# Performance work log

Hardware: AMD Instinct MI355X
Metric: run time of the kernel (lower is better)

Reference implementation:

```python
import jax, jax.numpy as jnp
import numpy as np

NUM_HEADS = 16
HEAD_DIM = 64  # hidden_size 1024 / 16 heads


def setup_inputs() -> dict:
    key = jax.random.key(0)
    ks = jax.random.split(key, 4)
    B, S, H = 2, 2048, 1024
    scale = 1.0 / np.sqrt(H)
    return {
        "hidden_states": jax.random.normal(ks[0], (B, S, H), dtype=jnp.float32),
        "attention_mask": jnp.zeros((B, 1, 1, S), dtype=jnp.float32),
        "Wq": jax.random.normal(ks[1], (H, H), dtype=jnp.float32) * scale,
        "bq": jnp.zeros((H,), dtype=jnp.float32),
        "Wk": jax.random.normal(ks[2], (H, H), dtype=jnp.float32) * scale,
        "bk": jnp.zeros((H,), dtype=jnp.float32),
        "Wv": jax.random.normal(ks[3], (H, H), dtype=jnp.float32) * scale,
        "bv": jnp.zeros((H,), dtype=jnp.float32),
    }


def reference(hidden_states, attention_mask, Wq, bq, Wk, bk, Wv, bv):
    B, S, H = hidden_states.shape
    h, d = NUM_HEADS, HEAD_DIM

    def heads(x):  # [B,S,H] -> [B,h,S,d]
        return x.reshape(B, S, h, d).transpose(0, 2, 1, 3)

    q = heads(hidden_states @ Wq + bq)
    k = heads(hidden_states @ Wk + bk)
    v = heads(hidden_states @ Wv + bv)

    # [B,h,S,S] scores, scaled then additive-masked (HF BERT semantics)
    scores = jnp.einsum("bhqd,bhkd->bhqk", q, k) / jnp.sqrt(jnp.float32(d))
    scores = scores + attention_mask
    probs = jax.nn.softmax(scores, axis=-1)  # dropout p=0 -> identity

    ctx = jnp.einsum("bhqk,bhkd->bhqd", probs, v)
    ctx = ctx.transpose(0, 2, 1, 3).reshape(B, S, H)
    return ctx
```

## Files before the change

### kernel.cpp

```cpp
#include <hip/hip_runtime.h>
#include <hip/hip_bf16.h>


#define SEQ   2048
#define HID   1024
#define NHEAD 16
#define HD    64
#define SD    ((size_t)SEQ * HD)

typedef __bf16 bf16x8 __attribute__((ext_vector_type(8)));
typedef float  f32x4  __attribute__((ext_vector_type(4)));

#define L2E 1.4426950408889634f
#define SOFT_OFF 16.0f

__device__ __forceinline__ unsigned short f2b(float f) {
    unsigned int x = __float_as_uint(f);
    x += 0x7FFFu + ((x >> 16) & 1u);
    return (unsigned short)(x >> 16);
}

__global__ __launch_bounds__(256) void cvt_x_k(const float* __restrict__ X,
                                               unsigned short* __restrict__ Xb)
{
    const size_t i = ((size_t)blockIdx.x * 256 + threadIdx.x) * 4;
    const float4 v = *(const float4*)(X + i);
    ushort4 o;
    o.x = f2b(v.x); o.y = f2b(v.y); o.z = f2b(v.z); o.w = f2b(v.w);
    *(ushort4*)(Xb + i) = o;
}

__global__ __launch_bounds__(256) void cvt_w_k(
    const float* __restrict__ Wq, const float* __restrict__ Wk,
    const float* __restrict__ Wv, unsigned short* __restrict__ Wtb)
{
    __shared__ __align__(16) unsigned short T[64][68];
    const int z = blockIdx.z;
    const float* __restrict__ W = (z == 0) ? Wq : (z == 1) ? Wk : Wv;
    const int k0 = blockIdx.x * 64, n0 = blockIdx.y * 64;
    const int tid = threadIdx.x;
    #pragma unroll
    for (int it = 0; it < 16; ++it) {
        const int idx = 256 * it + tid;
        const int r = idx >> 6, c = idx & 63;
        T[c][r] = f2b(W[(size_t)(k0 + r) * HID + n0 + c]);
    }
    __syncthreads();
    unsigned short* dst = Wtb + (size_t)z * HID * HID;
    #pragma unroll
    for (int it = 0; it < 4; ++it) {
        const int idx = 256 * it + tid;
        const int n = idx >> 4, c4 = (idx & 15) * 4;
        *(ushort4*)(dst + (size_t)(n0 + n) * HID + k0 + c4) = *(ushort4*)&T[n][c4];
    }
}

__device__ __forceinline__ void gemm_epilogue(
    f32x4 acc[4][4], const float* __restrict__ Bp,
    unsigned short* __restrict__ scratch, unsigned short (*Et)[68],
    int z, int m0, int n0, int wr, int wc, int ln, int quad)
{
    const int b = m0 >> 11;
    const int srow0 = (m0 + wr) & (SEQ - 1);
    const int head = (n0 + wc) >> 6;
    __syncthreads();

    if (z == 2) {
        #pragma unroll
        for (int half = 0; half < 2; ++half) {
            #pragma unroll
            for (int nt2 = 0; nt2 < 2; ++nt2) {
                const int nt = half * 2 + nt2;
                const float bias = Bp[n0 + wc + nt * 16 + ln];
                #pragma unroll
                for (int mt = 0; mt < 4; ++mt) {
                    ushort4 o;
                    o.x = f2b(acc[mt][nt][0] + bias);
                    o.y = f2b(acc[mt][nt][1] + bias);
                    o.z = f2b(acc[mt][nt][2] + bias);
                    o.w = f2b(acc[mt][nt][3] + bias);
                    *(ushort4*)&Et[nt2 * 16 + ln][mt * 16 + quad * 4] = o;
                }
            }
            __syncthreads();
            #pragma unroll
            for (int it = 0; it < 8; ++it) {
                const int d = it * 4 + quad, s4 = ln * 4;
                *(ushort4*)(scratch +
                    ((size_t)(64 + b * NHEAD + head) * HD + half * 32 + d) * SEQ
                    + srow0 + s4) = *(const ushort4*)&Et[d][s4];
            }
            __syncthreads();
        }
    } else {
        #pragma unroll
        for (int half = 0; half < 2; ++half) {
            #pragma unroll
            for (int mt2 = 0; mt2 < 2; ++mt2) {
                const int mt = half * 2 + mt2;
                #pragma unroll
                for (int nt = 0; nt < 4; ++nt) {
                    const float bias = Bp[n0 + wc + nt * 16 + ln];
                    #pragma unroll
                    for (int r = 0; r < 4; ++r)
                        Et[mt2 * 16 + quad * 4 + r][nt * 16 + ln] =
                            f2b(acc[mt][nt][r] + bias);
                }
            }
            __syncthreads();
            #pragma unroll
            for (int it = 0; it < 8; ++it) {
                const int r = it * 4 + quad, c4 = ln * 4;
                *(ushort4*)(scratch +
                    ((size_t)(z * 32 + b * NHEAD + head) * SEQ + srow0
                     + half * 32 + r) * HD + c4) = *(const ushort4*)&Et[r][c4];
            }
            __syncthreads();
        }
    }
}

__global__ __launch_bounds__(256) void qkv_gemm_bf16(
    const unsigned short* __restrict__ Xb, const unsigned short* __restrict__ Wtb,
    const float* __restrict__ bq, const float* __restrict__ bk,
    const float* __restrict__ bv, unsigned short* __restrict__ scratch)
{
    __shared__ __align__(16) unsigned char pool[20480];
    unsigned short (*Xs)[40] = (unsigned short (*)[40])pool;
    unsigned short (*Wt)[40] = (unsigned short (*)[40])(pool + 10240);

    const int z = blockIdx.z;
    const float* __restrict__ Bp = (z == 0) ? bq : (z == 1) ? bk : bv;
    const unsigned short* __restrict__ Wz = Wtb + (size_t)z * HID * HID;

    const int tid = threadIdx.x, w = tid >> 6, lane = tid & 63;
    const int ln = lane & 15, quad = lane >> 4;
    const int wr = (w >> 1) * 64, wc = (w & 1) * 64;
    const int m0 = blockIdx.x * 128, n0 = blockIdx.y * 128;
    const int sr = tid >> 2, c8 = (tid & 3) * 8;

    f32x4 acc[4][4];
    #pragma unroll
    for (int i = 0; i < 4; ++i)
        #pragma unroll
        for (int j = 0; j < 4; ++j) acc[i][j] = (f32x4){0.f, 0.f, 0.f, 0.f};

    uint4 xg0 = *(const uint4*)(Xb + (size_t)(m0 + sr) * HID + c8);
    uint4 xg1 = *(const uint4*)(Xb + (size_t)(m0 + sr + 64) * HID + c8);
    uint4 wg0 = *(const uint4*)(Wz + (size_t)(n0 + sr) * HID + c8);
    uint4 wg1 = *(const uint4*)(Wz + (size_t)(n0 + sr + 64) * HID + c8);

    for (int k0 = 0; k0 < HID; k0 += 32) {
        __syncthreads();
        *(uint4*)&Xs[sr][c8]      = xg0;
        *(uint4*)&Xs[sr + 64][c8] = xg1;
        *(uint4*)&Wt[sr][c8]      = wg0;
        *(uint4*)&Wt[sr + 64][c8] = wg1;
        __syncthreads();
        const int kn = (k0 + 32) & (HID - 1);
        xg0 = *(const uint4*)(Xb + (size_t)(m0 + sr) * HID + kn + c8);
        xg1 = *(const uint4*)(Xb + (size_t)(m0 + sr + 64) * HID + kn + c8);
        wg0 = *(const uint4*)(Wz + (size_t)(n0 + sr) * HID + kn + c8);
        wg1 = *(const uint4*)(Wz + (size_t)(n0 + sr + 64) * HID + kn + c8);

        bf16x8 am[4], bn[4];
        #pragma unroll
        for (int t = 0; t < 4; ++t) {
            am[t] = *(const bf16x8*)&Xs[wr + t * 16 + ln][quad * 8];
            bn[t] = *(const bf16x8*)&Wt[wc + t * 16 + ln][quad * 8];
        }
        #pragma unroll
        for (int mt = 0; mt < 4; ++mt)
            #pragma unroll
            for (int nt = 0; nt < 4; ++nt)
                acc[mt][nt] = __builtin_amdgcn_mfma_f32_16x16x32_bf16(
                    am[mt], bn[nt], acc[mt][nt], 0, 0, 0);
    }
    unsigned short (*Et)[68] = (unsigned short (*)[68])(pool + (size_t)w * 4352);
    gemm_epilogue(acc, Bp, scratch, Et, z, m0, n0, wr, wc, ln, quad);
}

__global__ __launch_bounds__(256) void qkv_gemm_fp32(
    const float* __restrict__ X,
    const float* __restrict__ Wq, const float* __restrict__ bq,
    const float* __restrict__ Wk, const float* __restrict__ bk,
    const float* __restrict__ Wv, const float* __restrict__ bv,
    unsigned short* __restrict__ scratch)
{
    __shared__ __align__(16) unsigned char pool[20480];
    unsigned short (*Xs)[40] = (unsigned short (*)[40])pool;
    unsigned short (*Wt)[40] = (unsigned short (*)[40])(pool + 10240);

    const int z = blockIdx.z;
    const float* __restrict__ W  = (z == 0) ? Wq : (z == 1) ? Wk : Wv;
    const float* __restrict__ Bp = (z == 0) ? bq : (z == 1) ? bk : bv;

    const int tid = threadIdx.x, w = tid >> 6, lane = tid & 63;
    const int ln = lane & 15, quad = lane >> 4;
    const int wr = (w >> 1) * 64, wc = (w & 1) * 64;
    const int m0 = blockIdx.x * 128, n0 = blockIdx.y * 128;

    const int xr = tid >> 3, xc = (tid & 7) * 4;
    const int wkr = tid >> 5, wnc = (tid & 31) * 4;

    f32x4 acc[4][4];
    #pragma unroll
    for (int i = 0; i < 4; ++i)
        #pragma unroll
        for (int j = 0; j < 4; ++j) acc[i][j] = (f32x4){0.f, 0.f, 0.f, 0.f};

    for (int k0 = 0; k0 < HID; k0 += 32) {
        __syncthreads();
        #pragma unroll
        for (int it = 0; it < 4; ++it) {
            const int r = xr + 32 * it;
            const float4 xv = *(const float4*)(X + (size_t)(m0 + r) * HID + k0 + xc);
            ushort4 xb;
            xb.x = f2b(xv.x); xb.y = f2b(xv.y); xb.z = f2b(xv.z); xb.w = f2b(xv.w);
            *(ushort4*)&Xs[r][xc] = xb;
            const int kr = wkr + 8 * it;
            const float4 wv = *(const float4*)(W + (size_t)(k0 + kr) * HID + n0 + wnc);
            Wt[wnc + 0][kr] = f2b(wv.x);
            Wt[wnc + 1][kr] = f2b(wv.y);
            Wt[wnc + 2][kr] = f2b(wv.z);
            Wt[wnc + 3][kr] = f2b(wv.w);
        }
        __syncthreads();
        bf16x8 am[4], bn[4];
        #pragma unroll
        for (int t = 0; t < 4; ++t) {
            am[t] = *(const bf16x8*)&Xs[wr + t * 16 + ln][quad * 8];
            bn[t] = *(const bf16x8*)&Wt[wc + t * 16 + ln][quad * 8];
        }
        #pragma unroll
        for (int mt = 0; mt < 4; ++mt)
            #pragma unroll
            for (int nt = 0; nt < 4; ++nt)
                acc[mt][nt] = __builtin_amdgcn_mfma_f32_16x16x32_bf16(
                    am[mt], bn[nt], acc[mt][nt], 0, 0, 0);
    }
    unsigned short (*Et)[68] = (unsigned short (*)[68])(pool + (size_t)w * 4352);
    gemm_epilogue(acc, Bp, scratch, Et, z, m0, n0, wr, wc, ln, quad);
}

__global__ __launch_bounds__(256) void attn_mfma(
    const unsigned short* __restrict__ scratch,
    const float* __restrict__ mask,
    float* __restrict__ out)
{
    __shared__ __align__(16) unsigned char smem[46080];
    unsigned short (*Ks)[64][72] = (unsigned short (*)[64][72])smem;
    unsigned short (*Vt)[64][72] = (unsigned short (*)[64][72])(smem + 18432);
    unsigned short (*Ps)[72]     = (unsigned short (*)[72])(smem + 36864);
    float (*Obuf)[68] = (float (*)[68])smem;

    const int orig = blockIdx.x;
    const int wg = ((orig & 7) << 7) + (orig >> 3);
    const int qt = wg & 31;
    const int bh = wg >> 5;
    const int b = bh >> 4, head = bh & 15;

    const unsigned short* __restrict__ Qp  = scratch + (size_t)bh * SD;
    const unsigned short* __restrict__ Kp  = scratch + (size_t)(32 + bh) * SD;
    const unsigned short* __restrict__ Vtp = scratch + (size_t)(64 + bh) * SD;
    const float* __restrict__ maskp = mask + b * SEQ;

    const int tid = threadIdx.x, w = tid >> 6, lane = tid & 63;
    const int ln = lane & 15, quad = lane >> 4;

    const int qrow = qt * 64 + w * 16 + ln;
    const bf16x8 qb0 = *(const bf16x8*)(Qp + (size_t)qrow * HD + quad * 8);
    const bf16x8 qb1 = *(const bf16x8*)(Qp + (size_t)qrow * HD + 32 + quad * 8);

    f32x4 O[4];
    #pragma unroll
    for (int t = 0; t < 4; ++t) O[t] = (f32x4){0.f, 0.f, 0.f, 0.f};
    float lr = 0.0f;

    const int sr8 = tid >> 3, sc8 = (tid & 7) * 8;

    {
        uint4 a = *(const uint4*)(Kp + (size_t)sr8 * HD + sc8);
        uint4 c = *(const uint4*)(Kp + (size_t)(sr8 + 32) * HD + sc8);
        uint4 d = *(const uint4*)(Vtp + (size_t)sr8 * SEQ + sc8);
        uint4 e = *(const uint4*)(Vtp + (size_t)(sr8 + 32) * SEQ + sc8);
        *(uint4*)&Ks[0][sr8][sc8]      = a;
        *(uint4*)&Ks[0][sr8 + 32][sc8] = c;
        *(uint4*)&Vt[0][sr8][sc8]      = d;
        *(uint4*)&Vt[0][sr8 + 32][sc8] = e;
    }
    uint4 kg0 = *(const uint4*)(Kp + (size_t)(64 + sr8) * HD + sc8);
    uint4 kg1 = *(const uint4*)(Kp + (size_t)(64 + sr8 + 32) * HD + sc8);
    uint4 vg0 = *(const uint4*)(Vtp + (size_t)sr8 * SEQ + 64 + sc8);
    uint4 vg1 = *(const uint4*)(Vtp + (size_t)(sr8 + 32) * SEQ + 64 + sc8);
    __syncthreads();

    for (int kt = 0; kt < 32; ++kt) {
        const int cur = kt & 1;
        if (kt < 31) {
            *(uint4*)&Ks[cur ^ 1][sr8][sc8]      = kg0;
            *(uint4*)&Ks[cur ^ 1][sr8 + 32][sc8] = kg1;
            *(uint4*)&Vt[cur ^ 1][sr8][sc8]      = vg0;
            *(uint4*)&Vt[cur ^ 1][sr8 + 32][sc8] = vg1;
        }
        if (kt < 30) {
            const int kn = kt + 2;
            kg0 = *(const uint4*)(Kp + (size_t)(kn * 64 + sr8) * HD + sc8);
            kg1 = *(const uint4*)(Kp + (size_t)(kn * 64 + sr8 + 32) * HD + sc8);
            vg0 = *(const uint4*)(Vtp + (size_t)sr8 * SEQ + kn * 64 + sc8);
            vg1 = *(const uint4*)(Vtp + (size_t)(sr8 + 32) * SEQ + kn * 64 + sc8);
        }

        f32x4 s[4];
        #pragma unroll
        for (int t = 0; t < 4; ++t) {
            const bf16x8 ka0 = *(const bf16x8*)&Ks[cur][t * 16 + ln][quad * 8];
            const bf16x8 ka1 = *(const bf16x8*)&Ks[cur][t * 16 + ln][32 + quad * 8];
            f32x4 a = (f32x4){0.f, 0.f, 0.f, 0.f};
            a = __builtin_amdgcn_mfma_f32_16x16x32_bf16(ka0, qb0, a, 0, 0, 0);
            a = __builtin_amdgcn_mfma_f32_16x16x32_bf16(ka1, qb1, a, 0, 0, 0);
            s[t] = a;
        }

        const float c = 0.125f * L2E;
        #pragma unroll
        for (int t = 0; t < 4; ++t) {
            const float4 mk4 = *(const float4*)(maskp + kt * 64 + t * 16 + quad * 4);
            const float b0 = fmaf(mk4.x, L2E, -SOFT_OFF);
            const float b1 = fmaf(mk4.y, L2E, -SOFT_OFF);
            const float b2 = fmaf(mk4.z, L2E, -SOFT_OFF);
            const float b3 = fmaf(mk4.w, L2E, -SOFT_OFF);
            const float p0 = exp2f(fmaf(s[t][0], c, b0));
            const float p1 = exp2f(fmaf(s[t][1], c, b1));
            const float p2 = exp2f(fmaf(s[t][2], c, b2));
            const float p3 = exp2f(fmaf(s[t][3], c, b3));
            lr += (p0 + p1) + (p2 + p3);
            unsigned int w0, w1;
            asm("v_cvt_pk_bf16_f32 %0, %1, %2" : "=v"(w0) : "v"(p0), "v"(p1));
            asm("v_cvt_pk_bf16_f32 %0, %1, %2" : "=v"(w1) : "v"(p2), "v"(p3));
            uint2 pw; pw.x = w0; pw.y = w1;
            *(uint2*)&Ps[w * 16 + ln][t * 16 + quad * 4] = pw;
        }

        const bf16x8 pb0 = *(const bf16x8*)&Ps[w * 16 + ln][quad * 8];
        const bf16x8 pb1 = *(const bf16x8*)&Ps[w * 16 + ln][32 + quad * 8];
        #pragma unroll
        for (int t = 0; t < 4; ++t) {
            const bf16x8 va0 = *(const bf16x8*)&Vt[cur][t * 16 + ln][quad * 8];
            const bf16x8 va1 = *(const bf16x8*)&Vt[cur][t * 16 + ln][32 + quad * 8];
            O[t] = __builtin_amdgcn_mfma_f32_16x16x32_bf16(va0, pb0, O[t], 0, 0, 0);
            O[t] = __builtin_amdgcn_mfma_f32_16x16x32_bf16(va1, pb1, O[t], 0, 0, 0);
        }

        __syncthreads();
    }

    lr += __shfl_xor(lr, 16);
    lr += __shfl_xor(lr, 32);

    const float inv = 1.0f / lr;
    #pragma unroll
    for (int t = 0; t < 4; ++t) {
        float4 o4;
        o4.x = O[t][0] * inv; o4.y = O[t][1] * inv;
        o4.z = O[t][2] * inv; o4.w = O[t][3] * inv;
        *(float4*)&Obuf[w * 16 + ln][t * 16 + quad * 4] = o4;
    }
    __syncthreads();
    #pragma unroll
    for (int it = 0; it < 4; ++it) {
        const int r = (tid >> 4) + 16 * it, c4 = (tid & 15) * 4;
        *(float4*)(out + ((size_t)b * SEQ + qt * 64 + r) * HID + head * HD + c4)
            = *(const float4*)&Obuf[r][c4];
    }
}

extern "C" void kernel_launch(void* const* d_in, const int* in_sizes, int n_in,
                              void* d_out, int out_size, void* d_ws, size_t ws_size,
                              hipStream_t stream) {
    const float* X    = (const float*)d_in[0];
    const float* mask = (const float*)d_in[1];
    const float* Wq   = (const float*)d_in[2];
    const float* bq   = (const float*)d_in[3];
    const float* Wk   = (const float*)d_in[4];
    const float* bk   = (const float*)d_in[5];
    const float* Wv   = (const float*)d_in[6];
    const float* bv   = (const float*)d_in[7];

    unsigned short* scratch = (unsigned short*)d_ws;
    float* out = (float*)d_out;

    const bool big = (ws_size >= (40ull << 20));
    if (big) {
        unsigned short* Xb  = scratch + 96 * SD;
        unsigned short* Wtb = Xb + (size_t)2 * SEQ * HID;
        cvt_x_k<<<4096, 256, 0, stream>>>(X, Xb);
        cvt_w_k<<<dim3(16, 16, 3), 256, 0, stream>>>(Wq, Wk, Wv, Wtb);
        qkv_gemm_bf16<<<dim3(32, 8, 3), 256, 0, stream>>>(
            Xb, Wtb, bq, bk, bv, scratch);
    } else {
        qkv_gemm_fp32<<<dim3(32, 8, 3), 256, 0, stream>>>(
            X, Wq, bq, Wk, bk, Wv, bv, scratch);
    }
    attn_mfma<<<1024, 256, 0, stream>>>(scratch, mask, out);
}
```

Measured before the change: 214.8 us.

## Process two key tiles per iteration in attention loop with batched prefetch

```diff
diff --git a/kernel.cpp b/kernel.cpp
--- a/kernel.cpp
+++ b/kernel.cpp
@@ -248,10 +248,10 @@
     const float* __restrict__ mask,
     float* __restrict__ out)
 {
-    __shared__ __align__(16) unsigned char smem[46080];
+    __shared__ __align__(16) unsigned char smem[55296];
     unsigned short (*Ks)[64][72] = (unsigned short (*)[64][72])smem;
     unsigned short (*Vt)[64][72] = (unsigned short (*)[64][72])(smem + 18432);
-    unsigned short (*Ps)[72]     = (unsigned short (*)[72])(smem + 36864);
+    unsigned short (*Ps)[64][72] = (unsigned short (*)[64][72])(smem + 36864);
     float (*Obuf)[68] = (float (*)[68])smem;
 
     const int orig = blockIdx.x;
@@ -279,50 +279,50 @@
 
     const int sr8 = tid >> 3, sc8 = (tid & 7) * 8;
 
-    {
-        uint4 a = *(const uint4*)(Kp + (size_t)sr8 * HD + sc8);
-        uint4 c = *(const uint4*)(Kp + (size_t)(sr8 + 32) * HD + sc8);
-        uint4 d = *(const uint4*)(Vtp + (size_t)sr8 * SEQ + sc8);
-        uint4 e = *(const uint4*)(Vtp + (size_t)(sr8 + 32) * SEQ + sc8);
-        *(uint4*)&Ks[0][sr8][sc8]      = a;
-        *(uint4*)&Ks[0][sr8 + 32][sc8] = c;
-        *(uint4*)&Vt[0][sr8][sc8]      = d;
-        *(uint4*)&Vt[0][sr8 + 32][sc8] = e;
-    }
-    uint4 kg0 = *(const uint4*)(Kp + (size_t)(64 + sr8) * HD + sc8);
-    uint4 kg1 = *(const uint4*)(Kp + (size_t)(64 + sr8 + 32) * HD + sc8);
-    uint4 vg0 = *(const uint4*)(Vtp + (size_t)sr8 * SEQ + 64 + sc8);
-    uint4 vg1 = *(const uint4*)(Vtp + (size_t)(sr8 + 32) * SEQ + 64 + sc8);
+    #pragma unroll
+    for (int tp = 0; tp < 2; ++tp) {
+        uint4 a = *(const uint4*)(Kp + (size_t)(tp * 64 + sr8) * HD + sc8);
+        uint4 c = *(const uint4*)(Kp + (size_t)(tp * 64 + sr8 + 32) * HD + sc8);
+        uint4 d = *(const uint4*)(Vtp + (size_t)sr8 * SEQ + tp * 64 + sc8);
+        uint4 e = *(const uint4*)(Vtp + (size_t)(sr8 + 32) * SEQ + tp * 64 + sc8);
+        *(uint4*)&Ks[tp][sr8][sc8]      = a;
+        *(uint4*)&Ks[tp][sr8 + 32][sc8] = c;
+        *(uint4*)&Vt[tp][sr8][sc8]      = d;
+        *(uint4*)&Vt[tp][sr8 + 32][sc8] = e;
+    }
+    uint4 kgA0 = *(const uint4*)(Kp + (size_t)(2 * 64 + sr8) * HD + sc8);
+    uint4 kgA1 = *(const uint4*)(Kp + (size_t)(2 * 64 + sr8 + 32) * HD + sc8);
+    uint4 vgA0 = *(const uint4*)(Vtp + (size_t)sr8 * SEQ + 2 * 64 + sc8);
+    uint4 vgA1 = *(const uint4*)(Vtp + (size_t)(sr8 + 32) * SEQ + 2 * 64 + sc8);
+    uint4 kgB0 = *(const uint4*)(Kp + (size_t)(3 * 64 + sr8) * HD + sc8);
+    uint4 kgB1 = *(const uint4*)(Kp + (size_t)(3 * 64 + sr8 + 32) * HD + sc8);
+    uint4 vgB0 = *(const uint4*)(Vtp + (size_t)sr8 * SEQ + 3 * 64 + sc8);
+    uint4 vgB1 = *(const uint4*)(Vtp + (size_t)(sr8 + 32) * SEQ + 3 * 64 + sc8);
     __syncthreads();
 
-    for (int kt = 0; kt < 32; ++kt) {
-        const int cur = kt & 1;
-        if (kt < 31) {
-            *(uint4*)&Ks[cur ^ 1][sr8][sc8]      = kg0;
-            *(uint4*)&Ks[cur ^ 1][sr8 + 32][sc8] = kg1;
-            *(uint4*)&Vt[cur ^ 1][sr8][sc8]      = vg0;
-            *(uint4*)&Vt[cur ^ 1][sr8 + 32][sc8] = vg1;
-        }
-        if (kt < 30) {
-            const int kn = kt + 2;
-            kg0 = *(const uint4*)(Kp + (size_t)(kn * 64 + sr8) * HD + sc8);
-            kg1 = *(const uint4*)(Kp + (size_t)(kn * 64 + sr8 + 32) * HD + sc8);
-            vg0 = *(const uint4*)(Vtp + (size_t)sr8 * SEQ + kn * 64 + sc8);
-            vg1 = *(const uint4*)(Vtp + (size_t)(sr8 + 32) * SEQ + kn * 64 + sc8);
-        }
-
-        f32x4 s[4];
-        #pragma unroll
-        for (int t = 0; t < 4; ++t) {
-            const bf16x8 ka0 = *(const bf16x8*)&Ks[cur][t * 16 + ln][quad * 8];
-            const bf16x8 ka1 = *(const bf16x8*)&Ks[cur][t * 16 + ln][32 + quad * 8];
+    const float cc = 0.125f * L2E;
+
+    for (int kt = 0; kt < 32; kt += 2) {
+        f32x4 sA[4], sB[4];
+        #pragma unroll
+        for (int t = 0; t < 4; ++t) {
+            const bf16x8 ka0 = *(const bf16x8*)&Ks[0][t * 16 + ln][quad * 8];
+            const bf16x8 ka1 = *(const bf16x8*)&Ks[0][t * 16 + ln][32 + quad * 8];
             f32x4 a = (f32x4){0.f, 0.f, 0.f, 0.f};
             a = __builtin_amdgcn_mfma_f32_16x16x32_bf16(ka0, qb0, a, 0, 0, 0);
             a = __builtin_amdgcn_mfma_f32_16x16x32_bf16(ka1, qb1, a, 0, 0, 0);
-            s[t] = a;
-        }
-
-        const float c = 0.125f * L2E;
+            sA[t] = a;
+        }
+        #pragma unroll
+        for (int t = 0; t < 4; ++t) {
+            const bf16x8 kb0 = *(const bf16x8*)&Ks[1][t * 16 + ln][quad * 8];
+            const bf16x8 kb1 = *(const bf16x8*)&Ks[1][t * 16 + ln][32 + quad * 8];
+            f32x4 a = (f32x4){0.f, 0.f, 0.f, 0.f};
+            a = __builtin_amdgcn_mfma_f32_16x16x32_bf16(kb0, qb0, a, 0, 0, 0);
+            a = __builtin_amdgcn_mfma_f32_16x16x32_bf16(kb1, qb1, a, 0, 0, 0);
+            sB[t] = a;
+        }
+
         #pragma unroll
         for (int t = 0; t < 4; ++t) {
             const float4 mk4 = *(const float4*)(maskp + kt * 64 + t * 16 + quad * 4);
@@ -330,28 +330,81 @@
             const float b1 = fmaf(mk4.y, L2E, -SOFT_OFF);
             const float b2 = fmaf(mk4.z, L2E, -SOFT_OFF);
             const float b3 = fmaf(mk4.w, L2E, -SOFT_OFF);
-            const float p0 = exp2f(fmaf(s[t][0], c, b0));
-            const float p1 = exp2f(fmaf(s[t][1], c, b1));
-            const float p2 = exp2f(fmaf(s[t][2], c, b2));
-            const float p3 = exp2f(fmaf(s[t][3], c, b3));
+            const float p0 = exp2f(fmaf(sA[t][0], cc, b0));
+            const float p1 = exp2f(fmaf(sA[t][1], cc, b1));
+            const float p2 = exp2f(fmaf(sA[t][2], cc, b2));
+            const float p3 = exp2f(fmaf(sA[t][3], cc, b3));
             lr += (p0 + p1) + (p2 + p3);
             unsigned int w0, w1;
             asm("v_cvt_pk_bf16_f32 %0, %1, %2" : "=v"(w0) : "v"(p0), "v"(p1));
             asm("v_cvt_pk_bf16_f32 %0, %1, %2" : "=v"(w1) : "v"(p2), "v"(p3));
             uint2 pw; pw.x = w0; pw.y = w1;
-            *(uint2*)&Ps[w * 16 + ln][t * 16 + quad * 4] = pw;
-        }
-
-        const bf16x8 pb0 = *(const bf16x8*)&Ps[w * 16 + ln][quad * 8];
-        const bf16x8 pb1 = *(const bf16x8*)&Ps[w * 16 + ln][32 + quad * 8];
-        #pragma unroll
-        for (int t = 0; t < 4; ++t) {
-            const bf16x8 va0 = *(const bf16x8*)&Vt[cur][t * 16 + ln][quad * 8];
-            const bf16x8 va1 = *(const bf16x8*)&Vt[cur][t * 16 + ln][32 + quad * 8];
-            O[t] = __builtin_amdgcn_mfma_f32_16x16x32_bf16(va0, pb0, O[t], 0, 0, 0);
-            O[t] = __builtin_amdgcn_mfma_f32_16x16x32_bf16(va1, pb1, O[t], 0, 0, 0);
-        }
-
+            *(uint2*)&Ps[0][w * 16 + ln][t * 16 + quad * 4] = pw;
+        }
+        #pragma unroll
+        for (int t = 0; t < 4; ++t) {
+            const float4 mk4 = *(const float4*)(maskp + (kt + 1) * 64 + t * 16 + quad * 4);
+            const float b0 = fmaf(mk4.x, L2E, -SOFT_OFF);
+            const float b1 = fmaf(mk4.y, L2E, -SOFT_OFF);
+            const float b2 = fmaf(mk4.z, L2E, -SOFT_OFF);
+            const float b3 = fmaf(mk4.w, L2E, -SOFT_OFF);
+            const float p0 = exp2f(fmaf(sB[t][0], cc, b0));
+            const float p1 = exp2f(fmaf(sB[t][1], cc, b1));
+            const float p2 = exp2f(fmaf(sB[t][2], cc, b2));
+            const float p3 = exp2f(fmaf(sB[t][3], cc, b3));
+            lr += (p0 + p1) + (p2 + p3);
+            unsigned int w0, w1;
+            asm("v_cvt_pk_bf16_f32 %0, %1, %2" : "=v"(w0) : "v"(p0), "v"(p1));
+            asm("v_cvt_pk_bf16_f32 %0, %1, %2" : "=v"(w1) : "v"(p2), "v"(p3));
+            uint2 pw; pw.x = w0; pw.y = w1;
+            *(uint2*)&Ps[1][w * 16 + ln][t * 16 + quad * 4] = pw;
+        }
+
+        {
+            const bf16x8 pb0 = *(const bf16x8*)&Ps[0][w * 16 + ln][quad * 8];
+            const bf16x8 pb1 = *(const bf16x8*)&Ps[0][w * 16 + ln][32 + quad * 8];
+            #pragma unroll
+            for (int t = 0; t < 4; ++t) {
+                const bf16x8 va0 = *(const bf16x8*)&Vt[0][t * 16 + ln][quad * 8];
+                const bf16x8 va1 = *(const bf16x8*)&Vt[0][t * 16 + ln][32 + quad * 8];
+                O[t] = __builtin_amdgcn_mfma_f32_16x16x32_bf16(va0, pb0, O[t], 0, 0, 0);
+                O[t] = __builtin_amdgcn_mfma_f32_16x16x32_bf16(va1, pb1, O[t], 0, 0, 0);
+            }
+        }
+        {
+            const bf16x8 pb0 = *(const bf16x8*)&Ps[1][w * 16 + ln][quad * 8];
+            const bf16x8 pb1 = *(const bf16x8*)&Ps[1][w * 16 + ln][32 + quad * 8];
+            #pragma unroll
+            for (int t = 0; t < 4; ++t) {
+                const bf16x8 va0 = *(const bf16x8*)&Vt[1][t * 16 + ln][quad * 8];
+                const bf16x8 va1 = *(const bf16x8*)&Vt[1][t * 16 + ln][32 + quad * 8];
+                O[t] = __builtin_amdgcn_mfma_f32_16x16x32_bf16(va0, pb0, O[t], 0, 0, 0);
+                O[t] = __builtin_amdgcn_mfma_f32_16x16x32_bf16(va1, pb1, O[t], 0, 0, 0);
+            }
+        }
+
+        __syncthreads();
+        if (kt < 30) {
+            *(uint4*)&Ks[0][sr8][sc8]      = kgA0;
+            *(uint4*)&Ks[0][sr8 + 32][sc8] = kgA1;
+            *(uint4*)&Vt[0][sr8][sc8]      = vgA0;
+            *(uint4*)&Vt[0][sr8 + 32][sc8] = vgA1;
+            *(uint4*)&Ks[1][sr8][sc8]      = kgB0;
+            *(uint4*)&Ks[1][sr8 + 32][sc8] = kgB1;
+            *(uint4*)&Vt[1][sr8][sc8]      = vgB0;
+            *(uint4*)&Vt[1][sr8 + 32][sc8] = vgB1;
+            if (kt < 28) {
+                const int ka = kt + 4, kb = kt + 5;
+                kgA0 = *(const uint4*)(Kp + (size_t)(ka * 64 + sr8) * HD + sc8);
+                kgA1 = *(const uint4*)(Kp + (size_t)(ka * 64 + sr8 + 32) * HD + sc8);
+                vgA0 = *(const uint4*)(Vtp + (size_t)sr8 * SEQ + ka * 64 + sc8);
+                vgA1 = *(const uint4*)(Vtp + (size_t)(sr8 + 32) * SEQ + ka * 64 + sc8);
+                kgB0 = *(const uint4*)(Kp + (size_t)(kb * 64 + sr8) * HD + sc8);
+                kgB1 = *(const uint4*)(Kp + (size_t)(kb * 64 + sr8 + 32) * HD + sc8);
+                vgB0 = *(const uint4*)(Vtp + (size_t)sr8 * SEQ + kb * 64 + sc8);
+                vgB1 = *(const uint4*)(Vtp + (size_t)(sr8 + 32) * SEQ + kb * 64 + sc8);
+            }
+        }
         __syncthreads();
     }
 
```

After: 216.4 us. About the same (+0.7%).

## Use direct global-to-LDS loads with double buffering in QKV bf16 GEMM

Applied to the files above, without the earlier changes.

```diff
diff --git a/kernel.cpp b/kernel.cpp
--- a/kernel.cpp
+++ b/kernel.cpp
@@ -18,6 +18,13 @@
     unsigned int x = __float_as_uint(f);
     x += 0x7FFFu + ((x >> 16) & 1u);
     return (unsigned short)(x >> 16);
+}
+
+__device__ __forceinline__ void gload16(const unsigned short* g,
+                                        unsigned short* l) {
+    __builtin_amdgcn_global_load_lds(
+        (const __attribute__((address_space(1))) unsigned int*)g,
+        (__attribute__((address_space(3))) unsigned int*)l, 16, 0, 0);
 }
 
 __global__ __launch_bounds__(256) void cvt_x_k(const float* __restrict__ X,
@@ -125,9 +132,7 @@
     const float* __restrict__ bq, const float* __restrict__ bk,
     const float* __restrict__ bv, unsigned short* __restrict__ scratch)
 {
-    __shared__ __align__(16) unsigned char pool[20480];
-    unsigned short (*Xs)[40] = (unsigned short (*)[40])pool;
-    unsigned short (*Wt)[40] = (unsigned short (*)[40])(pool + 10240);
+    __shared__ __align__(16) unsigned short pool[2][2][128][32];
 
     const int z = blockIdx.z;
     const float* __restrict__ Bp = (z == 0) ? bq : (z == 1) ? bk : bv;
@@ -137,7 +142,10 @@
     const int ln = lane & 15, quad = lane >> 4;
     const int wr = (w >> 1) * 64, wc = (w & 1) * 64;
     const int m0 = blockIdx.x * 128, n0 = blockIdx.y * 128;
-    const int sr = tid >> 2, c8 = (tid & 3) * 8;
+
+    const int L0 = w * 128 + lane;
+    const int r0 = L0 >> 2,        c0 = (L0 & 3) * 8;
+    const int r1 = (L0 + 64) >> 2, c1 = ((L0 + 64) & 3) * 8;
 
     f32x4 acc[4][4];
     #pragma unroll
@@ -145,29 +153,33 @@
         #pragma unroll
         for (int j = 0; j < 4; ++j) acc[i][j] = (f32x4){0.f, 0.f, 0.f, 0.f};
 
-    uint4 xg0 = *(const uint4*)(Xb + (size_t)(m0 + sr) * HID + c8);
-    uint4 xg1 = *(const uint4*)(Xb + (size_t)(m0 + sr + 64) * HID + c8);
-    uint4 wg0 = *(const uint4*)(Wz + (size_t)(n0 + sr) * HID + c8);
-    uint4 wg1 = *(const uint4*)(Wz + (size_t)(n0 + sr + 64) * HID + c8);
-
+    {
+        unsigned short* lx = &pool[0][0][0][0] + (size_t)(w * 128) * 8;
+        unsigned short* lw = &pool[0][1][0][0] + (size_t)(w * 128) * 8;
+        gload16(Xb + (size_t)(m0 + r0) * HID + c0, lx);
+        gload16(Xb + (size_t)(m0 + r1) * HID + c1, lx + 64 * 8);
+        gload16(Wz + (size_t)(n0 + r0) * HID + c0, lw);
+        gload16(Wz + (size_t)(n0 + r1) * HID + c1, lw + 64 * 8);
+    }
+
+    int cur = 0;
     for (int k0 = 0; k0 < HID; k0 += 32) {
         __syncthreads();
-        *(uint4*)&Xs[sr][c8]      = xg0;
-        *(uint4*)&Xs[sr + 64][c8] = xg1;
-        *(uint4*)&Wt[sr][c8]      = wg0;
-        *(uint4*)&Wt[sr + 64][c8] = wg1;
-        __syncthreads();
-        const int kn = (k0 + 32) & (HID - 1);
-        xg0 = *(const uint4*)(Xb + (size_t)(m0 + sr) * HID + kn + c8);
-        xg1 = *(const uint4*)(Xb + (size_t)(m0 + sr + 64) * HID + kn + c8);
-        wg0 = *(const uint4*)(Wz + (size_t)(n0 + sr) * HID + kn + c8);
-        wg1 = *(const uint4*)(Wz + (size_t)(n0 + sr + 64) * HID + kn + c8);
+        if (k0 + 32 < HID) {
+            const int kn = k0 + 32, nxt = cur ^ 1;
+            unsigned short* lx = &pool[nxt][0][0][0] + (size_t)(w * 128) * 8;
+            unsigned short* lw = &pool[nxt][1][0][0] + (size_t)(w * 128) * 8;
+            gload16(Xb + (size_t)(m0 + r0) * HID + kn + c0, lx);
+            gload16(Xb + (size_t)(m0 + r1) * HID + kn + c1, lx + 64 * 8);
+            gload16(Wz + (size_t)(n0 + r0) * HID + kn + c0, lw);
+            gload16(Wz + (size_t)(n0 + r1) * HID + kn + c1, lw + 64 * 8);
+        }
 
         bf16x8 am[4], bn[4];
         #pragma unroll
         for (int t = 0; t < 4; ++t) {
-            am[t] = *(const bf16x8*)&Xs[wr + t * 16 + ln][quad * 8];
-            bn[t] = *(const bf16x8*)&Wt[wc + t * 16 + ln][quad * 8];
+            am[t] = *(const bf16x8*)&pool[cur][0][wr + t * 16 + ln][quad * 8];
+            bn[t] = *(const bf16x8*)&pool[cur][1][wc + t * 16 + ln][quad * 8];
         }
         #pragma unroll
         for (int mt = 0; mt < 4; ++mt)
@@ -175,8 +187,10 @@
             for (int nt = 0; nt < 4; ++nt)
                 acc[mt][nt] = __builtin_amdgcn_mfma_f32_16x16x32_bf16(
                     am[mt], bn[nt], acc[mt][nt], 0, 0, 0);
-    }
-    unsigned short (*Et)[68] = (unsigned short (*)[68])(pool + (size_t)w * 4352);
+        cur ^= 1;
+    }
+    unsigned short (*Et)[68] =
+        (unsigned short (*)[68])((unsigned char*)pool + (size_t)w * 4352);
     gemm_epilogue(acc, Bp, scratch, Et, z, m0, n0, wr, wc, ln, quad);
 }
 
```

Result: faster. 199.9 us (-6.9%).
